# Performance work log

Hardware: AMD Instinct MI355X
Metric: run time of the kernel (lower is better)

The kernel has to match this reference:

```python
import jax, jax.numpy as jnp
import numpy as np

N = 30000   # nodes
E = 480000  # edges
C = 64      # in_channels
NC = 101    # num_classes
K1 = 5      # kernel_size per dim
K = K1 * K1 # 25 kernel weight matrices (dim=2)


def _spline_conv(x, src, dst, pseudo, W, root, bias):
    """SplineConv, degree-1 open B-spline, dim=2, kernel_size=5, aggr='mean'.
    x: [N,C_in], pseudo: [E,2] in [0,1], W: [25,C_in,C_out], root: [C_in,C_out].
    """
    n, c = x.shape
    v = pseudo * (K1 - 1)                       # [E,2] in [0, K1-1]
    bot = jnp.clip(jnp.floor(v), 0, K1 - 1)
    frac = v - bot                              # fractional part
    bot_i = bot.astype(jnp.int32)
    bits = jnp.array([[0, 0], [0, 1], [1, 0], [1, 1]], dtype=jnp.int32)  # S=4 combos
    idx_d = jnp.clip(bot_i[:, None, :] + bits[None, :, :], 0, K1 - 1)    # [E,4,2]
    w_d = jnp.where(bits[None, :, :] == 1, frac[:, None, :], 1.0 - frac[:, None, :])
    B = w_d[..., 0] * w_d[..., 1]               # [E,4] basis weights
    kidx = idx_d[..., 0] * K1 + idx_d[..., 1]   # [E,4] flat kernel index in [0,25)
    msg = B[:, :, None] * x[src][:, None, :]    # [E,4,C] weighted source feats
    seg = (dst[:, None] * K + kidx).reshape(-1) # combined (node,kernel) segment id
    acc = jax.ops.segment_sum(msg.reshape(-1, c), seg, num_segments=n * K)
    acc = acc.reshape(n, K, c)                  # [N,25,C]
    out = jnp.einsum('nkc,kcd->nd', acc, W)     # apply kernel weight matrices
    deg = jax.ops.segment_sum(jnp.ones(dst.shape[0], x.dtype), dst, num_segments=n)
    out = out / jnp.maximum(deg, 1.0)[:, None]  # mean aggregation
    out = out + x @ root                        # root weight
    if bias is not None:
        out = out + bias
    return out


def _bn(x, g, b):
    m = x.mean(0)
    v = x.var(0)
    return g * (x - m) * jax.lax.rsqrt(v + 1e-5) + b


def setup_inputs() -> dict:
    key = jax.random.key(0)
    ks = jax.random.split(key, 30)
    p = lambda k, shape: jax.random.normal(k, shape, jnp.float32) * 0.05
    d = {
        'x': jax.random.normal(ks[0], (N, C), jnp.float32),
        'edge_attr': jax.random.uniform(ks[1], (E, 3), dtype=jnp.float32),
        'src': jax.random.randint(ks[2], (E,), 0, N),
        'dst': jax.random.randint(ks[3], (E,), 0, N),
    }
    for i, name in enumerate(['conv1', 'conv2', 'conv3']):
        d[name + '_W'] = p(ks[4 + 2 * i], (K, C, C))
        d[name + '_root'] = p(ks[5 + 2 * i], (C, C))
        d['norm%d_gamma' % (i + 1)] = jnp.ones((C,), jnp.float32)
        d['norm%d_beta' % (i + 1)] = jnp.zeros((C,), jnp.float32)
    for j, (name, oc) in enumerate([('regr', 4), ('cls', NC), ('obj', 1)]):
        d[name + '_W'] = p(ks[10 + 3 * j], (K, C, oc))
        d[name + '_root'] = p(ks[11 + 3 * j], (C, oc))
        d[name + '_bias'] = jnp.zeros((oc,), jnp.float32)
    return d


def reference(x, edge_attr, src, dst,
              conv1_W, conv1_root, norm1_gamma, norm1_beta,
              conv2_W, conv2_root, norm2_gamma, norm2_beta,
              conv3_W, conv3_root, norm3_gamma, norm3_beta,
              regr_W, regr_root, regr_bias,
              cls_W, cls_root, cls_bias,
              obj_W, obj_root, obj_bias):
    pseudo = edge_attr[:, :2]
    x1 = jax.nn.relu(_bn(_spline_conv(x, src, dst, pseudo, conv1_W, conv1_root, None), norm1_gamma, norm1_beta))
    x2 = jax.nn.relu(_bn(_spline_conv(x1, src, dst, pseudo, conv2_W, conv2_root, None), norm2_gamma, norm2_beta))
    x3 = jax.nn.relu(_bn(_spline_conv(x1, src, dst, pseudo, conv3_W, conv3_root, None), norm3_gamma, norm3_beta))
    reg = _spline_conv(x2, src, dst, pseudo, regr_W, regr_root, regr_bias)
    cls = _spline_conv(x3, src, dst, pseudo, cls_W, cls_root, cls_bias)
    obj = _spline_conv(x3, src, dst, pseudo, obj_W, obj_root, obj_bias)
    return (cls, reg, obj)
```

## Files before the change

kernel.cpp:

```cpp
#include <hip/hip_runtime.h>
#include <hip/hip_bf16.h>

#define NN 30000
#define NE 480000
#define CIN 64
#define KD 1600
#define KT 1664
#define KMAC 13
#define BM 32
#define NBLK 938
#define MROWS (NBLK*BM)
#define NBS 118
#define REG_OFF  (30000*101)
#define OBJ_OFF  (30000*105)

typedef short bf16x8 __attribute__((ext_vector_type(8)));
typedef float f32x4  __attribute__((ext_vector_type(4)));

__device__ __forceinline__ ushort f2bf(float x) {
    union { float f; unsigned u; } v; v.f = x;
    unsigned r = v.u + 0x7FFFu + ((v.u >> 16) & 1u);
    return (ushort)(r >> 16);
}

__global__ void k_count(const int* __restrict__ dst, int* __restrict__ deg) {
    int e = blockIdx.x * 256 + threadIdx.x;
    if (e < NE) atomicAdd(&deg[dst[e]], 1);
}

__global__ void k_scan1(const int* __restrict__ deg, int* __restrict__ bsum) {
    __shared__ int sred[4];
    int i = blockIdx.x * 256 + threadIdx.x;
    int v = (i < NN) ? deg[i] : 0;
    #pragma unroll
    for (int o = 32; o >= 1; o >>= 1) v += __shfl_down(v, o);
    int w = threadIdx.x >> 6, l = threadIdx.x & 63;
    if (l == 0) sred[w] = v;
    __syncthreads();
    if (threadIdx.x == 0) bsum[blockIdx.x] = sred[0] + sred[1] + sred[2] + sred[3];
}

__global__ void k_scan2(const int* __restrict__ bsum, int* __restrict__ boff) {
    __shared__ int s[128];
    int t = threadIdx.x;
    int v = (t < NBS) ? bsum[t] : 0;
    s[t] = v; __syncthreads();
    for (int o = 1; o < 128; o <<= 1) {
        int u = (t >= o) ? s[t - o] : 0;
        __syncthreads(); s[t] += u; __syncthreads();
    }
    if (t < NBS) boff[t] = s[t] - v;
}

__global__ void k_scan3(const int* __restrict__ deg, const int* __restrict__ boff,
                        int* __restrict__ rp, int* __restrict__ cur, float* __restrict__ invd) {
    __shared__ int s[256];
    int t = threadIdx.x;
    int i = blockIdx.x * 256 + t;
    int v = (i < NN) ? deg[i] : 0;
    s[t] = v; __syncthreads();
    for (int o = 1; o < 256; o <<= 1) {
        int u = (t >= o) ? s[t - o] : 0;
        __syncthreads(); s[t] += u; __syncthreads();
    }
    int ex = s[t] - v + boff[blockIdx.x];
    if (i < NN) {
        rp[i] = ex; cur[i] = ex;
        invd[i] = 1.f / (float)(v > 0 ? v : 1);
    }
    if (i == NN - 1) rp[NN] = NE;
}

__global__ void k_scatter(const float* __restrict__ ea, const int* __restrict__ src,
                          const int* __restrict__ dst, int* __restrict__ cur,
                          float4* __restrict__ mB, int2* __restrict__ mI) {
    int e = blockIdx.x * 256 + threadIdx.x;
    if (e >= NE) return;
    float p0 = ea[e*3+0], p1 = ea[e*3+1];
    float v0 = p0*4.f, v1 = p1*4.f;
    float b0 = fminf(fmaxf(floorf(v0),0.f),4.f);
    float b1 = fminf(fmaxf(floorf(v1),0.f),4.f);
    float f0 = v0-b0, f1 = v1-b1;
    int i0 = (int)b0, i1 = (int)b1;
    float B00 = (1.f-f0)*(1.f-f1);
    float B01 = (1.f-f0)*f1;
    float B10 = f0*(1.f-f1);
    float B11 = f0*f1;
    int k00 = i0*5 + i1;
    int dn = dst[e];
    int pos = atomicAdd(&cur[dn], 1);
    mB[pos] = make_float4(B00,B01,B10,B11);
    mI[pos] = make_int2(k00, src[e]);
}

__global__ void k_prepw(const float* W1,const float* R1,const float* W2,const float* R2,
                        const float* W3,const float* R3,const float* Wr,const float* Rr,
                        const float* Wc,const float* Rc,const float* Wo,const float* Ro,
                        ushort* T1, ushort* T23, ushort* Tr, ushort* TcTo) {
    int b = blockIdx.x;
    const float* W; const float* R; ushort* T; int od; int col;
    if      (b < 64)  { W=W1; R=R1; T=T1  + (long)b*KT;       od=64;  col=b;     }
    else if (b < 128) { W=W2; R=R2; T=T23 + (long)(b-64)*KT;  od=64;  col=b-64;  }
    else if (b < 192) { W=W3; R=R3; T=T23 + (long)(b-64)*KT;  od=64;  col=b-128; }
    else if (b < 208) { W=Wr; R=Rr; T=Tr  + (long)(b-192)*KT; od=4;   col=b-192; }
    else if (b < 320) { W=Wc; R=Rc; T=TcTo+ (long)(b-208)*KT; od=101; col=b-208; }
    else              { W=Wo; R=Ro; T=TcTo+ (long)(b-208)*KT; od=1;   col=b-320; }
    for (int kc = threadIdx.x; kc < KT; kc += 256) {
        float v = 0.f;
        if (col < od) v = (kc < KD) ? W[(long)kc*od + col] : R[(long)(kc-KD)*od + col];
        T[kc] = f2bf(v);
    }
}

#define AGGC(K, A_, B_, C_, D_) case K: A_ += bb.x*xu; B_ += bb.y*xu; C_ += bb.z*xu; D_ += bb.w*xu; break;

template<bool NORM>
__global__ void k_agg(const int* __restrict__ rp, const float4* __restrict__ mB,
                      const int2* __restrict__ mI, const float* __restrict__ f,
                      const float* __restrict__ invd,
                      const float* __restrict__ st, const float* __restrict__ g,
                      const float* __restrict__ be, ushort* __restrict__ A) {
    int wid = (blockIdx.x * 256 + threadIdx.x) >> 6;
    wid = __builtin_amdgcn_readfirstlane(wid);
    int l = threadIdx.x & 63;
    if (wid >= NN) return;
    float na = 0.f, nc = 0.f;
    if (NORM) {
        const float inv_n = 1.f / (float)NN;
        float mm = st[l] * inv_n;
        float var = st[64 + l] * inv_n - mm * mm;
        float rs = rsqrtf(var + 1e-5f);
        na = g[l] * rs; nc = be[l] - mm * na;
    }
    float a00=0.f,a01=0.f,a02=0.f,a03=0.f,a04=0.f;
    float a05=0.f,a06=0.f,a07=0.f,a08=0.f,a09=0.f;
    float a10=0.f,a11=0.f,a12=0.f,a13=0.f,a14=0.f;
    float a15=0.f,a16=0.f,a17=0.f,a18=0.f,a19=0.f;
    float a20=0.f,a21=0.f,a22=0.f,a23=0.f,a24=0.f;
    int beg = rp[wid], end = rp[wid + 1];
    for (int e0 = beg; e0 < end; e0 += 8) {
        int2 m[8];
        #pragma unroll
        for (int u = 0; u < 8; ++u) {
            int e = e0 + u;
            m[u] = mI[(e < end) ? e : beg];
        }
        float xv[8];
        #pragma unroll
        for (int u = 0; u < 8; ++u) xv[u] = f[(long)m[u].y * CIN + l];
        __builtin_amdgcn_sched_barrier(0);
        float4 b[8];
        #pragma unroll
        for (int u = 0; u < 8; ++u) {
            int e = e0 + u;
            b[u] = mB[(e < end) ? e : beg];
            if (e >= end) b[u] = make_float4(0,0,0,0);
        }
        __builtin_amdgcn_sched_barrier(0);
        #pragma unroll
        for (int u = 0; u < 8; ++u) {
            float xu = xv[u];
            if (NORM) xu = fmaxf(xu * na + nc, 0.f);
            int k00 = __builtin_amdgcn_readfirstlane(m[u].x);
            float4 bb = b[u];
            switch (k00) {
                AGGC(0,  a00,a01,a05,a06)
                AGGC(1,  a01,a02,a06,a07)
                AGGC(2,  a02,a03,a07,a08)
                AGGC(3,  a03,a04,a08,a09)
                AGGC(5,  a05,a06,a10,a11)
                AGGC(6,  a06,a07,a11,a12)
                AGGC(7,  a07,a08,a12,a13)
                AGGC(8,  a08,a09,a13,a14)
                AGGC(10, a10,a11,a15,a16)
                AGGC(11, a11,a12,a16,a17)
                AGGC(12, a12,a13,a17,a18)
                AGGC(13, a13,a14,a18,a19)
                AGGC(15, a15,a16,a20,a21)
                AGGC(16, a16,a17,a21,a22)
                AGGC(17, a17,a18,a22,a23)
                AGGC(18, a18,a19,a23,a24)
                default: break;
            }
        }
    }
    float s = invd[wid];
    ushort* rb = A + (long)wid * KT + l;
    #define STO(K, V) rb[K*CIN] = f2bf((V) * s);
    STO(0,a00)  STO(1,a01)  STO(2,a02)  STO(3,a03)  STO(4,a04)
    STO(5,a05)  STO(6,a06)  STO(7,a07)  STO(8,a08)  STO(9,a09)
    STO(10,a10) STO(11,a11) STO(12,a12) STO(13,a13) STO(14,a14)
    STO(15,a15) STO(16,a16) STO(17,a17) STO(18,a18) STO(19,a19)
    STO(20,a20) STO(21,a21) STO(22,a22) STO(23,a23) STO(24,a24)
    #undef STO
    float rv = f[(long)wid * CIN + l];
    if (NORM) rv = fmaxf(rv * na + nc, 0.f);
    rb[KD] = f2bf(rv);
}

template<int MODE>
__global__ void k_gemm(const ushort* __restrict__ A, const ushort* __restrict__ B,
                       float* __restrict__ o0, float* __restrict__ o1,
                       float* __restrict__ s0, float* __restrict__ s1,
                       const float* __restrict__ b0, const float* __restrict__ b1) {
    __shared__ ushort As[2 * 4096];
    f32x4* part = (f32x4*)As;
    const int tid = threadIdx.x, w = tid >> 6, l = tid & 63;
    const int m0 = blockIdx.x * BM;

    int colrow;
    if constexpr (MODE == 0)      colrow = ((w & 3) << 4) + (l & 15);
    else if constexpr (MODE == 2) colrow = (l & 15);
    else                          colrow = (w << 4) + (l & 15);
    const ushort* Bp = B + (long)colrow * KT + ((l >> 4) << 3);

    const int r0 = tid >> 4, j0 = tid & 15;
    const ushort* Asrc = A + (long)(m0 + r0) * KT + (j0 << 3);
    const int swzo = ((j0 ^ (r0 & 7)) << 4);

    f32x4 acc[2];
    acc[0] = (f32x4){0.f,0.f,0.f,0.f};
    acc[1] = (f32x4){0.f,0.f,0.f,0.f};

    *(int4*)((char*)As + r0 * 256 + swzo) = *(const int4*)(Asrc);
    __syncthreads();

    int buf = 0;
    for (int ks = 0; ks < KMAC; ++ks) {
        int4 vn;
        if (ks < KMAC - 1) vn = *(const int4*)(Asrc + (ks + 1) * 128);
        bool act;
        if constexpr (MODE == 0)      act = (w < 4) ? (ks < 7) : (ks >= 7);
        else if constexpr (MODE == 2) act = ((ks & 7) == w);
        else                          act = true;
        if (act) {
            const char* Ab = (const char*)As + buf * 8192;
            #pragma unroll
            for (int s = 0; s < 4; ++s) {
                bf16x8 bb = *(const bf16x8*)(Bp + ks * 128 + s * 32);
                #pragma unroll
                for (int m = 0; m < 2; ++m) {
                    int r = (m << 4) + (l & 15);
                    int j = (s << 2) + (l >> 4);
                    bf16x8 a = *(const bf16x8*)(Ab + r * 256 + ((j ^ (r & 7)) << 4));
                    acc[m] = __builtin_amdgcn_mfma_f32_16x16x32_bf16(a, bb, acc[m], 0, 0, 0);
                }
            }
        }
        if (ks < KMAC - 1)
            *(int4*)((char*)As + (buf ^ 1) * 8192 + r0 * 256 + swzo) = vn;
        __syncthreads();
        buf ^= 1;
    }

    auto emit = [&](f32x4* ac, float* out, int ostride, int col, int odcap, float bv, float* stats) {
        float p1 = 0.f, p2 = 0.f;
        #pragma unroll
        for (int m = 0; m < 2; ++m) {
            #pragma unroll
            for (int r = 0; r < 4; ++r) {
                int row = m0 + (m << 4) + ((l >> 4) << 2) + r;
                if (row < NN) {
                    float v = ac[m][r] + bv;
                    if (col < odcap) out[(long)row * ostride + col] = v;
                    p1 += v; p2 += v * v;
                }
            }
        }
        if (stats) {
            p1 += __shfl_down(p1, 32); p2 += __shfl_down(p2, 32);
            p1 += __shfl_down(p1, 16); p2 += __shfl_down(p2, 16);
            if (l < 16) { atomicAdd(&stats[col], p1); atomicAdd(&stats[64 + col], p2); }
        }
    };

    if constexpr (MODE == 0) {
        if (w >= 4) {
            #pragma unroll
            for (int m = 0; m < 2; ++m) part[((w & 3) << 7) + (l << 1) + m] = acc[m];
        }
        __syncthreads();
        if (w < 4) {
            #pragma unroll
            for (int m = 0; m < 2; ++m) acc[m] += part[((w & 3) << 7) + (l << 1) + m];
            emit(acc, o0, 64, ((w & 3) << 4) + (l & 15), 64, 0.f, s0);
        }
    } else if constexpr (MODE == 1) {
        if (w < 4) emit(acc, o0, 64, (w << 4) + (l & 15), 64, 0.f, s0);
        else       emit(acc, o1, 64, ((w - 4) << 4) + (l & 15), 64, 0.f, s1);
    } else if constexpr (MODE == 2) {
        if (w > 0) {
            #pragma unroll
            for (int m = 0; m < 2; ++m) part[((w - 1) << 7) + (l << 1) + m] = acc[m];
        }
        __syncthreads();
        if (w == 0) {
            for (int i = 0; i < 7; ++i) {
                #pragma unroll
                for (int m = 0; m < 2; ++m) acc[m] += part[(i << 7) + (l << 1) + m];
            }
            int col = l & 15;
            emit(acc, o0, 4, col, 4, (col < 4) ? b0[col] : 0.f, nullptr);
        }
    } else {
        if (w < 7) {
            int col = (w << 4) + (l & 15);
            emit(acc, o0, 101, col, 101, (col < 101) ? b0[col] : 0.f, nullptr);
        } else {
            int col = l & 15;
            emit(acc, o1, 1, col, 1, b1[0], nullptr);
        }
    }
}

extern "C" void kernel_launch(void* const* d_in, const int* in_sizes, int n_in,
                              void* d_out, int out_size, void* d_ws, size_t ws_size,
                              hipStream_t stream) {
    const float* x    = (const float*)d_in[0];
    const float* ea   = (const float*)d_in[1];
    const int*   src  = (const int*)d_in[2];
    const int*   dst  = (const int*)d_in[3];
    const float* W1   = (const float*)d_in[4];
    const float* R1   = (const float*)d_in[5];
    const float* g1   = (const float*)d_in[6];
    const float* be1  = (const float*)d_in[7];
    const float* W2   = (const float*)d_in[8];
    const float* R2   = (const float*)d_in[9];
    const float* g2   = (const float*)d_in[10];
    const float* be2  = (const float*)d_in[11];
    const float* W3   = (const float*)d_in[12];
    const float* R3   = (const float*)d_in[13];
    const float* g3   = (const float*)d_in[14];
    const float* be3  = (const float*)d_in[15];
    const float* Wr   = (const float*)d_in[16];
    const float* Rr   = (const float*)d_in[17];
    const float* br   = (const float*)d_in[18];
    const float* Wc   = (const float*)d_in[19];
    const float* Rc   = (const float*)d_in[20];
    const float* bc   = (const float*)d_in[21];
    const float* Wo   = (const float*)d_in[22];
    const float* Ro   = (const float*)d_in[23];
    const float* bo   = (const float*)d_in[24];
    float* out = (float*)d_out;

    char* p = (char*)d_ws;
    auto alloc = [&](size_t bytes) { char* r = p; p += (bytes + 255) & ~(size_t)255; return r; };
    float4* mB   = (float4*)alloc((size_t)NE * 16);
    int2*   mI   = (int2*)  alloc((size_t)NE * 8);
    int*    deg  = (int*)   alloc((size_t)NN * 4);
    int*    rp   = (int*)   alloc((size_t)(NN + 1) * 4);
    int*    cur  = (int*)   alloc((size_t)NN * 4);
    float*  invd = (float*) alloc((size_t)NN * 4);
    int*    bsum = (int*)   alloc((size_t)NBS * 4);
    int*    boff = (int*)   alloc((size_t)NBS * 4);
    ushort* T1   = (ushort*)alloc((size_t)64  * KT * 2);
    ushort* T23  = (ushort*)alloc((size_t)128 * KT * 2);
    ushort* Tr   = (ushort*)alloc((size_t)16  * KT * 2);
    ushort* TcTo = (ushort*)alloc((size_t)128 * KT * 2);
    float*  y1   = (float*) alloc((size_t)NN * CIN * 4);
    float*  y2   = (float*) alloc((size_t)NN * CIN * 4);
    float*  y3   = (float*) alloc((size_t)NN * CIN * 4);
    float*  stats= (float*) alloc(3 * 128 * 4);
    ushort* A    = (ushort*)alloc((size_t)MROWS * KT * 2);
    float* st1 = stats, *st2 = stats + 128, *st3 = stats + 256;

    hipMemsetAsync(deg, 0, (size_t)NN * 4, stream);
    hipMemsetAsync(stats, 0, 3 * 128 * 4, stream);

    k_count  <<<1875, 256, 0, stream>>>(dst, deg);
    k_scan1  <<<NBS, 256, 0, stream>>>(deg, bsum);
    k_scan2  <<<1, 128, 0, stream>>>(bsum, boff);
    k_scan3  <<<NBS, 256, 0, stream>>>(deg, boff, rp, cur, invd);
    k_scatter<<<1875, 256, 0, stream>>>(ea, src, dst, cur, mB, mI);
    k_prepw  <<<336, 256, 0, stream>>>(W1,R1,W2,R2,W3,R3,Wr,Rr,Wc,Rc,Wo,Ro,T1,T23,Tr,TcTo);

    k_agg<false><<<7500, 256, 0, stream>>>(rp, mB, mI, x, invd, nullptr, nullptr, nullptr, A);
    k_gemm<0><<<NBLK, 512, 0, stream>>>(A, T1, y1, nullptr, st1, nullptr, nullptr, nullptr);
    k_agg<true><<<7500, 256, 0, stream>>>(rp, mB, mI, y1, invd, st1, g1, be1, A);
    k_gemm<1><<<NBLK, 512, 0, stream>>>(A, T23, y2, y3, st2, st3, nullptr, nullptr);
    k_agg<true><<<7500, 256, 0, stream>>>(rp, mB, mI, y2, invd, st2, g2, be2, A);
    k_gemm<2><<<NBLK, 512, 0, stream>>>(A, Tr, out + REG_OFF, nullptr, nullptr, nullptr, br, nullptr);
    k_agg<true><<<7500, 256, 0, stream>>>(rp, mB, mI, y3, invd, st3, g3, be3, A);
    k_gemm<3><<<NBLK, 512, 0, stream>>>(A, TcTo, out, out + OBJ_OFF, nullptr, nullptr, bc, bo);
}
```

Measured before the change: 450.2 us.

## Restructure GEMM to 16-row tiles with full-K LDS staging and 4 waves

The GEMM kernel now uses 16-row blocks with 256 threads, loads the whole 16x1664 A tile into LDS up front (about 53KB, with a 16-way XOR swizzle) instead of double-buffering 128-column slices with a barrier per step. Wave work is redistributed: in the modes with more output columns each wave computes two 16-column tiles, and the split-K reduction shrinks to 4 partial sums. This removes the per-step barriers and most of the cross-wave reductions, in exchange for higher LDS use per block, which limits occupancy, and fewer waves per block. NN divides evenly by 16, so the padded rows and their bounds checks are dropped.

```diff
diff --git a/kernel.cpp b/kernel.cpp
--- a/kernel.cpp
+++ b/kernel.cpp
@@ -7,9 +7,8 @@
 #define KD 1600
 #define KT 1664
 #define KMAC 13
-#define BM 32
-#define NBLK 938
-#define MROWS (NBLK*BM)
+#define BM 16
+#define NBLK 1875
 #define NBS 118
 #define REG_OFF  (30000*101)
 #define OBJ_OFF  (30000*105)
@@ -199,73 +198,48 @@
 }
 
 template<int MODE>
-__global__ void k_gemm(const ushort* __restrict__ A, const ushort* __restrict__ B,
+__global__ __launch_bounds__(256,3) void k_gemm(
+                       const ushort* __restrict__ A, const ushort* __restrict__ B,
                        float* __restrict__ o0, float* __restrict__ o1,
                        float* __restrict__ s0, float* __restrict__ s1,
                        const float* __restrict__ b0, const float* __restrict__ b1) {
-    __shared__ ushort As[2 * 4096];
+    __shared__ ushort As[BM * KT];
     f32x4* part = (f32x4*)As;
     const int tid = threadIdx.x, w = tid >> 6, l = tid & 63;
     const int m0 = blockIdx.x * BM;
 
-    int colrow;
-    if constexpr (MODE == 0)      colrow = ((w & 3) << 4) + (l & 15);
-    else if constexpr (MODE == 2) colrow = (l & 15);
-    else                          colrow = (w << 4) + (l & 15);
-    const ushort* Bp = B + (long)colrow * KT + ((l >> 4) << 3);
-
-    const int r0 = tid >> 4, j0 = tid & 15;
-    const ushort* Asrc = A + (long)(m0 + r0) * KT + (j0 << 3);
-    const int swzo = ((j0 ^ (r0 & 7)) << 4);
-
-    f32x4 acc[2];
-    acc[0] = (f32x4){0.f,0.f,0.f,0.f};
-    acc[1] = (f32x4){0.f,0.f,0.f,0.f};
-
-    *(int4*)((char*)As + r0 * 256 + swzo) = *(const int4*)(Asrc);
+    {
+        int4 v[13];
+        #pragma unroll
+        for (int i = 0; i < 13; ++i) {
+            int c = tid + (i << 8);
+            int row = c / 208, jj = c % 208;
+            v[i] = *(const int4*)(A + (long)(m0 + row) * KT + (jj << 3));
+        }
+        #pragma unroll
+        for (int i = 0; i < 13; ++i) {
+            int c = tid + (i << 8);
+            int row = c / 208, jj = c % 208;
+            int sw = jj ^ (row & 15);
+            *(int4*)((char*)As + row * 3328 + (sw << 4)) = v[i];
+        }
+    }
     __syncthreads();
 
-    int buf = 0;
-    for (int ks = 0; ks < KMAC; ++ks) {
-        int4 vn;
-        if (ks < KMAC - 1) vn = *(const int4*)(Asrc + (ks + 1) * 128);
-        bool act;
-        if constexpr (MODE == 0)      act = (w < 4) ? (ks < 7) : (ks >= 7);
-        else if constexpr (MODE == 2) act = ((ks & 7) == w);
-        else                          act = true;
-        if (act) {
-            const char* Ab = (const char*)As + buf * 8192;
-            #pragma unroll
-            for (int s = 0; s < 4; ++s) {
-                bf16x8 bb = *(const bf16x8*)(Bp + ks * 128 + s * 32);
-                #pragma unroll
-                for (int m = 0; m < 2; ++m) {
-                    int r = (m << 4) + (l & 15);
-                    int j = (s << 2) + (l >> 4);
-                    bf16x8 a = *(const bf16x8*)(Ab + r * 256 + ((j ^ (r & 7)) << 4));
-                    acc[m] = __builtin_amdgcn_mfma_f32_16x16x32_bf16(a, bb, acc[m], 0, 0, 0);
-                }
-            }
-        }
-        if (ks < KMAC - 1)
-            *(int4*)((char*)As + (buf ^ 1) * 8192 + r0 * 256 + swzo) = vn;
-        __syncthreads();
-        buf ^= 1;
-    }
-
-    auto emit = [&](f32x4* ac, float* out, int ostride, int col, int odcap, float bv, float* stats) {
+    auto lda = [&](int ks, int s) -> bf16x8 {
+        int r = l & 15;
+        int slot = (ks << 4) | ((((s << 2) | (l >> 4)) ^ r) & 15);
+        return *(const bf16x8*)((const char*)As + r * 3328 + (slot << 4));
+    };
+
+    auto emit = [&](f32x4 ac, float* out, int ostride, int col, int odcap, float bv, float* stats) {
         float p1 = 0.f, p2 = 0.f;
         #pragma unroll
-        for (int m = 0; m < 2; ++m) {
-            #pragma unroll
-            for (int r = 0; r < 4; ++r) {
-                int row = m0 + (m << 4) + ((l >> 4) << 2) + r;
-                if (row < NN) {
-                    float v = ac[m][r] + bv;
-                    if (col < odcap) out[(long)row * ostride + col] = v;
-                    p1 += v; p2 += v * v;
-                }
-            }
+        for (int r = 0; r < 4; ++r) {
+            int row = m0 + ((l >> 4) << 2) + r;
+            float v = ac[r] + bv;
+            if (col < odcap) out[(long)row * ostride + col] = v;
+            p1 += v; p2 += v * v;
         }
         if (stats) {
             p1 += __shfl_down(p1, 32); p2 += __shfl_down(p2, 32);
@@ -275,40 +249,69 @@
     };
 
     if constexpr (MODE == 0) {
-        if (w >= 4) {
+        const ushort* Bp = B + (long)((w << 4) + (l & 15)) * KT + ((l >> 4) << 3);
+        f32x4 acc = {0.f,0.f,0.f,0.f};
+        for (int ks = 0; ks < KMAC; ++ks) {
             #pragma unroll
-            for (int m = 0; m < 2; ++m) part[((w & 3) << 7) + (l << 1) + m] = acc[m];
+            for (int s = 0; s < 4; ++s) {
+                bf16x8 bb = *(const bf16x8*)(Bp + ks * 128 + s * 32);
+                acc = __builtin_amdgcn_mfma_f32_16x16x32_bf16(lda(ks, s), bb, acc, 0, 0, 0);
+            }
+        }
+        emit(acc, o0, 64, (w << 4) + (l & 15), 64, 0.f, s0);
+    } else if constexpr (MODE == 2) {
+        const ushort* Bp = B + (long)(l & 15) * KT + ((l >> 4) << 3);
+        int kb = (w * 13) >> 2, ke = ((w + 1) * 13) >> 2;
+        f32x4 acc = {0.f,0.f,0.f,0.f};
+        for (int ks = kb; ks < ke; ++ks) {
+            #pragma unroll
+            for (int s = 0; s < 4; ++s) {
+                bf16x8 bb = *(const bf16x8*)(Bp + ks * 128 + s * 32);
+                acc = __builtin_amdgcn_mfma_f32_16x16x32_bf16(lda(ks, s), bb, acc, 0, 0, 0);
+            }
         }
         __syncthreads();
-        if (w < 4) {
-            #pragma unroll
-            for (int m = 0; m < 2; ++m) acc[m] += part[((w & 3) << 7) + (l << 1) + m];
-            emit(acc, o0, 64, ((w & 3) << 4) + (l & 15), 64, 0.f, s0);
-        }
-    } else if constexpr (MODE == 1) {
-        if (w < 4) emit(acc, o0, 64, (w << 4) + (l & 15), 64, 0.f, s0);
-        else       emit(acc, o1, 64, ((w - 4) << 4) + (l & 15), 64, 0.f, s1);
-    } else if constexpr (MODE == 2) {
-        if (w > 0) {
-            #pragma unroll
-            for (int m = 0; m < 2; ++m) part[((w - 1) << 7) + (l << 1) + m] = acc[m];
-        }
+        part[(w << 6) + l] = acc;
         __syncthreads();
         if (w == 0) {
-            for (int i = 0; i < 7; ++i) {
-                #pragma unroll
-                for (int m = 0; m < 2; ++m) acc[m] += part[(i << 7) + (l << 1) + m];
-            }
+            f32x4 o = part[l];
+            #pragma unroll
+            for (int i = 1; i < 4; ++i) o += part[(i << 6) + l];
             int col = l & 15;
-            emit(acc, o0, 4, col, 4, (col < 4) ? b0[col] : 0.f, nullptr);
+            emit(o, o0, 4, col, 4, (col < 4) ? b0[col] : 0.f, nullptr);
         }
     } else {
-        if (w < 7) {
-            int col = (w << 4) + (l & 15);
-            emit(acc, o0, 101, col, 101, (col < 101) ? b0[col] : 0.f, nullptr);
+        int cb = w << 5;
+        const ushort* Bp0 = B + (long)(cb + (l & 15)) * KT + ((l >> 4) << 3);
+        const ushort* Bp1 = Bp0 + (long)16 * KT;
+        f32x4 ac0 = {0.f,0.f,0.f,0.f}, ac1 = {0.f,0.f,0.f,0.f};
+        for (int ks = 0; ks < KMAC; ++ks) {
+            #pragma unroll
+            for (int s = 0; s < 4; ++s) {
+                bf16x8 av = lda(ks, s);
+                bf16x8 bb0 = *(const bf16x8*)(Bp0 + ks * 128 + s * 32);
+                bf16x8 bb1 = *(const bf16x8*)(Bp1 + ks * 128 + s * 32);
+                ac0 = __builtin_amdgcn_mfma_f32_16x16x32_bf16(av, bb0, ac0, 0, 0, 0);
+                ac1 = __builtin_amdgcn_mfma_f32_16x16x32_bf16(av, bb1, ac1, 0, 0, 0);
+            }
+        }
+        if constexpr (MODE == 1) {
+            if (w < 2) {
+                emit(ac0, o0, 64, cb + (l & 15), 64, 0.f, s0);
+                emit(ac1, o0, 64, cb + 16 + (l & 15), 64, 0.f, s0);
+            } else {
+                emit(ac0, o1, 64, cb - 64 + (l & 15), 64, 0.f, s1);
+                emit(ac1, o1, 64, cb - 48 + (l & 15), 64, 0.f, s1);
+            }
         } else {
-            int col = l & 15;
-            emit(acc, o1, 1, col, 1, b1[0], nullptr);
+            int c0 = cb + (l & 15), c1 = cb + 16 + (l & 15);
+            if (w < 3) {
+                emit(ac0, o0, 101, c0, 101, (c0 < 101) ? b0[c0] : 0.f, nullptr);
+                emit(ac1, o0, 101, c1, 101, (c1 < 101) ? b0[c1] : 0.f, nullptr);
+            } else {
+                emit(ac0, o0, 101, c0, 101, (c0 < 101) ? b0[c0] : 0.f, nullptr);
+                emit(ac1, o1, 1, l & 15, 1, b1[0], nullptr);
+            }
         }
     }
 }
@@ -361,7 +364,7 @@
     float*  y2   = (float*) alloc((size_t)NN * CIN * 4);
     float*  y3   = (float*) alloc((size_t)NN * CIN * 4);
     float*  stats= (float*) alloc(3 * 128 * 4);
-    ushort* A    = (ushort*)alloc((size_t)MROWS * KT * 2);
+    ushort* A    = (ushort*)alloc((size_t)NN * KT * 2);
     float* st1 = stats, *st2 = stats + 128, *st3 = stats + 256;
 
     hipMemsetAsync(deg, 0, (size_t)NN * 4, stream);
@@ -375,11 +378,11 @@
     k_prepw  <<<336, 256, 0, stream>>>(W1,R1,W2,R2,W3,R3,Wr,Rr,Wc,Rc,Wo,Ro,T1,T23,Tr,TcTo);
 
     k_agg<false><<<7500, 256, 0, stream>>>(rp, mB, mI, x, invd, nullptr, nullptr, nullptr, A);
-    k_gemm<0><<<NBLK, 512, 0, stream>>>(A, T1, y1, nullptr, st1, nullptr, nullptr, nullptr);
+    k_gemm<0><<<NBLK, 256, 0, stream>>>(A, T1, y1, nullptr, st1, nullptr, nullptr, nullptr);
     k_agg<true><<<7500, 256, 0, stream>>>(rp, mB, mI, y1, invd, st1, g1, be1, A);
-    k_gemm<1><<<NBLK, 512, 0, stream>>>(A, T23, y2, y3, st2, st3, nullptr, nullptr);
+    k_gemm<1><<<NBLK, 256, 0, stream>>>(A, T23, y2, y3, st2, st3, nullptr, nullptr);
     k_agg<true><<<7500, 256, 0, stream>>>(rp, mB, mI, y2, invd, st2, g2, be2, A);
-    k_gemm<2><<<NBLK, 512, 0, stream>>>(A, Tr, out + REG_OFF, nullptr, nullptr, nullptr, br, nullptr);
+    k_gemm<2><<<NBLK, 256, 0, stream>>>(A, Tr, out + REG_OFF, nullptr, nullptr, nullptr, br, nullptr);
     k_agg<true><<<7500, 256, 0, stream>>>(rp, mB, mI, y3, invd, st3, g3, be3, A);
-    k_gemm<3><<<NBLK, 512, 0, stream>>>(A, TcTo, out, out + OBJ_OFF, nullptr, nullptr, bc, bo);
-}
+    k_gemm<3><<<NBLK, 256, 0, stream>>>(A, TcTo, out, out + OBJ_OFF, nullptr, nullptr, bc, bo);
+}
```

Measured after the change: 569.2 us. 26.4% more time.

## Double GEMM row tile and stage A tiles via direct global-to-LDS loads

Applied to the files above, without the earlier changes.

Raises the GEMM row tile from 32 to 64 rows per block, halving the block count, so each loaded B fragment feeds four MFMAs instead of two. The A-tile prefetch now uses global_load_lds to write straight into LDS, with the swizzle applied on the global source address instead of the LDS destination, removing the register round-trip. The cost is twice the LDS per block and more accumulator registers, which may lower occupancy. The grid of 469 blocks may also fill the GPU less evenly.

```diff
diff --git a/kernel.cpp b/kernel.cpp
--- a/kernel.cpp
+++ b/kernel.cpp
@@ -7,8 +7,8 @@
 #define KD 1600
 #define KT 1664
 #define KMAC 13
-#define BM 32
-#define NBLK 938
+#define BM 64
+#define NBLK 469
 #define MROWS (NBLK*BM)
 #define NBS 118
 #define REG_OFF  (30000*101)
@@ -16,6 +16,8 @@
 
 typedef short bf16x8 __attribute__((ext_vector_type(8)));
 typedef float f32x4  __attribute__((ext_vector_type(4)));
+typedef __attribute__((address_space(3))) unsigned lds_u32;
+typedef __attribute__((address_space(1))) const unsigned glb_u32;
 
 __device__ __forceinline__ ushort f2bf(float x) {
     union { float f; unsigned u; } v; v.f = x;
@@ -203,7 +205,7 @@
                        float* __restrict__ o0, float* __restrict__ o1,
                        float* __restrict__ s0, float* __restrict__ s1,
                        const float* __restrict__ b0, const float* __restrict__ b1) {
-    __shared__ ushort As[2 * 4096];
+    __shared__ ushort As[2 * 8192];
     f32x4* part = (f32x4*)As;
     const int tid = threadIdx.x, w = tid >> 6, l = tid & 63;
     const int m0 = blockIdx.x * BM;
@@ -214,32 +216,43 @@
     else                          colrow = (w << 4) + (l & 15);
     const ushort* Bp = B + (long)colrow * KT + ((l >> 4) << 3);
 
-    const int r0 = tid >> 4, j0 = tid & 15;
-    const ushort* Asrc = A + (long)(m0 + r0) * KT + (j0 << 3);
-    const int swzo = ((j0 ^ (r0 & 7)) << 4);
-
-    f32x4 acc[2];
-    acc[0] = (f32x4){0.f,0.f,0.f,0.f};
-    acc[1] = (f32x4){0.f,0.f,0.f,0.f};
-
-    *(int4*)((char*)As + r0 * 256 + swzo) = *(const int4*)(Asrc);
+    const int row0 = (w << 3) + (l >> 4);
+    const int row1 = row0 + 4;
+    const ushort* g0 = A + (long)(m0 + row0) * KT + (((l & 15) ^ (row0 & 7)) << 3);
+    const ushort* g1 = A + (long)(m0 + row1) * KT + (((l & 15) ^ (row1 & 7)) << 3);
+    ushort* d0 = (ushort*)As + (w << 10);
+    ushort* d1 = d0 + 512;
+
+    auto stage = [&](int ks, int bf) {
+        const ushort* sA = g0 + ks * 128;
+        const ushort* sB = g1 + ks * 128;
+        ushort* dA = d0 + (bf << 13);
+        ushort* dB = d1 + (bf << 13);
+        __builtin_amdgcn_global_load_lds((glb_u32*)sA, (lds_u32*)dA, 16, 0, 0);
+        __builtin_amdgcn_global_load_lds((glb_u32*)sB, (lds_u32*)dB, 16, 0, 0);
+    };
+
+    f32x4 acc[4];
+    #pragma unroll
+    for (int m = 0; m < 4; ++m) acc[m] = (f32x4){0.f,0.f,0.f,0.f};
+
+    stage(0, 0);
     __syncthreads();
 
     int buf = 0;
     for (int ks = 0; ks < KMAC; ++ks) {
-        int4 vn;
-        if (ks < KMAC - 1) vn = *(const int4*)(Asrc + (ks + 1) * 128);
+        if (ks < KMAC - 1) stage(ks + 1, buf ^ 1);
         bool act;
         if constexpr (MODE == 0)      act = (w < 4) ? (ks < 7) : (ks >= 7);
         else if constexpr (MODE == 2) act = ((ks & 7) == w);
         else                          act = true;
         if (act) {
-            const char* Ab = (const char*)As + buf * 8192;
+            const char* Ab = (const char*)As + buf * 16384;
             #pragma unroll
             for (int s = 0; s < 4; ++s) {
                 bf16x8 bb = *(const bf16x8*)(Bp + ks * 128 + s * 32);
                 #pragma unroll
-                for (int m = 0; m < 2; ++m) {
+                for (int m = 0; m < 4; ++m) {
                     int r = (m << 4) + (l & 15);
                     int j = (s << 2) + (l >> 4);
                     bf16x8 a = *(const bf16x8*)(Ab + r * 256 + ((j ^ (r & 7)) << 4));
@@ -247,8 +260,6 @@
                 }
             }
         }
-        if (ks < KMAC - 1)
-            *(int4*)((char*)As + (buf ^ 1) * 8192 + r0 * 256 + swzo) = vn;
         __syncthreads();
         buf ^= 1;
     }
@@ -256,7 +267,7 @@
     auto emit = [&](f32x4* ac, float* out, int ostride, int col, int odcap, float bv, float* stats) {
         float p1 = 0.f, p2 = 0.f;
         #pragma unroll
-        for (int m = 0; m < 2; ++m) {
+        for (int m = 0; m < 4; ++m) {
             #pragma unroll
             for (int r = 0; r < 4; ++r) {
                 int row = m0 + (m << 4) + ((l >> 4) << 2) + r;
@@ -277,12 +288,12 @@
     if constexpr (MODE == 0) {
         if (w >= 4) {
             #pragma unroll
-            for (int m = 0; m < 2; ++m) part[((w & 3) << 7) + (l << 1) + m] = acc[m];
+            for (int m = 0; m < 4; ++m) part[((w & 3) << 8) + (l << 2) + m] = acc[m];
         }
         __syncthreads();
         if (w < 4) {
             #pragma unroll
-            for (int m = 0; m < 2; ++m) acc[m] += part[((w & 3) << 7) + (l << 1) + m];
+            for (int m = 0; m < 4; ++m) acc[m] += part[((w & 3) << 8) + (l << 2) + m];
             emit(acc, o0, 64, ((w & 3) << 4) + (l & 15), 64, 0.f, s0);
         }
     } else if constexpr (MODE == 1) {
@@ -291,13 +302,13 @@
     } else if constexpr (MODE == 2) {
         if (w > 0) {
             #pragma unroll
-            for (int m = 0; m < 2; ++m) part[((w - 1) << 7) + (l << 1) + m] = acc[m];
+            for (int m = 0; m < 4; ++m) part[((w - 1) << 8) + (l << 2) + m] = acc[m];
         }
         __syncthreads();
         if (w == 0) {
             for (int i = 0; i < 7; ++i) {
                 #pragma unroll
-                for (int m = 0; m < 2; ++m) acc[m] += part[(i << 7) + (l << 1) + m];
+                for (int m = 0; m < 4; ++m) acc[m] += part[(i << 8) + (l << 2) + m];
             }
             int col = l & 15;
             emit(acc, o0, 4, col, 4, (col < 4) ? b0[col] : 0.f, nullptr);
```

New measurement: 392.4 us. -12.8%, faster.
